# Optimization experiments

Measured on AMD Instinct MI355X. Metric: run time of the kernel, lower is better.

Reference implementation:

```python
import jax, jax.numpy as jnp
import numpy as np
from jax import lax

SEQ_SIZE = 4096
V = 4                               # vocab size
B = 256                             # batch
FILTER_SIZES = [4, 5, 6, 7, 8]
H = 10                              # lstm hidden
I = (len(FILTER_SIZES) + 1) * V     # lstm input size = 24


def setup_inputs() -> dict:
    key = jax.random.key(0)
    ks = jax.random.split(key, 9)
    inp = {"x": jax.random.normal(ks[0], (B, 1, V * SEQ_SIZE), dtype=jnp.float32)}
    for fs in FILTER_SIZES:
        # matches nn.init.constant_(conv.weight, 0.01)
        inp[f"w{fs}"] = jnp.full((1, 1, fs), 0.01, dtype=jnp.float32)
    s = 1.0 / float(np.sqrt(H))
    shapes = {"Wih": (4 * H, I), "Whh": (4 * H, H), "bih": (4 * H,), "bhh": (4 * H,)}
    k = 1
    for d in ("f", "r"):
        for nm, sh in shapes.items():
            inp[f"{nm}_{d}"] = jax.random.uniform(ks[k], sh, jnp.float32, -s, s)
            k += 1
    return inp


def _branch(x, w, fs):
    # x: (B,1,V*S); conv1d stride=V, VALID, no bias -> (B,1,L)
    conv = lax.conv_general_dilated(x, w, window_strides=(V,), padding="VALID",
                                    dimension_numbers=("NCH", "OIH", "NCH"))
    # winner_takes_all: (x + max_over_len)^2
    m = jnp.max(conv, axis=2, keepdims=True)
    v = ((conv + m) ** 2)[:, 0, :]                                  # (B,L)
    Bsz, L = v.shape
    # shape_convolutions2 == scatter-add of v[b,i] into out[b, V*i + j], j<fs
    idx = (V * jnp.arange(L)[:, None] + jnp.arange(fs)[None, :]).reshape(-1)
    contrib = jnp.broadcast_to(v[:, :, None], (Bsz, L, fs)).reshape(Bsz, -1)
    out = jnp.zeros((Bsz, V * SEQ_SIZE), v.dtype).at[:, idx].add(contrib)
    return out.reshape(Bsz, SEQ_SIZE, V)


def _lstm_dir(xs, Wih, Whh, bih, bhh, reverse):
    # xs: (S,B,I) -> hidden states (S,B,H), aligned with input positions
    Bsz = xs.shape[1]
    h0 = jnp.zeros((Bsz, H), xs.dtype)
    c0 = jnp.zeros((Bsz, H), xs.dtype)
    b = bih + bhh

    def step(carry, xt):
        h, c = carry
        g = xt @ Wih.T + h @ Whh.T + b          # (B,4H), torch gate order i,f,g,o
        i, f, gg, o = jnp.split(g, 4, axis=1)
        c = jax.nn.sigmoid(f) * c + jax.nn.sigmoid(i) * jnp.tanh(gg)
        h = jax.nn.sigmoid(o) * jnp.tanh(c)
        return (h, c), h

    _, hs = lax.scan(step, (h0, c0), xs, reverse=reverse)
    return hs


def _forward(x, ws, Wih_f, Whh_f, bih_f, bhh_f, Wih_r, Whh_r, bih_r, bhh_r):
    Bsz = x.shape[0]
    branches = [_branch(x, w, fs) for w, fs in zip(ws, FILTER_SIZES)]
    inp_r = x.reshape(Bsz, SEQ_SIZE, V)
    l_lstmin = jnp.concatenate(branches + [inp_r], axis=2)   # (B,S,24)
    xs = jnp.swapaxes(l_lstmin, 0, 1)                        # (S,B,24)
    hf = _lstm_dir(xs, Wih_f, Whh_f, bih_f, bhh_f, False)
    hr = _lstm_dir(xs, Wih_r, Whh_r, bih_r, bhh_r, True)
    h_sum = jnp.sum(hf, axis=2) + jnp.sum(hr, axis=2)        # (S,B)
    h_sum = h_sum.T                                          # (B,S)
    # l_in * repeated h_sum, reshaped and summed over vocab == inp_r * h_sum
    l_profile = jnp.sum(inp_r * h_sum[:, :, None], axis=2)   # (B,S)
    return jax.nn.sigmoid(jnp.sum(l_profile, axis=1, keepdims=True))  # (B,1)


def reference(x, w4, w5, w6, w7, w8, Wih_f, Whh_f, bih_f, bhh_f, Wih_r, Whh_r, bih_r, bhh_r):
    return _forward(x, [w4, w5, w6, w7, w8],
                    Wih_f, Whh_f, bih_f, bhh_f, Wih_r, Whh_r, bih_r, bhh_r)
```

## Files before the change

kernel.cpp:

```cpp
#include <hip/hip_runtime.h>

#define SEQ 4096
#define NBATCH 256

typedef float v2f __attribute__((ext_vector_type(2)));

__device__ __forceinline__ float sqf(float v) { return v * v; }
__device__ __forceinline__ float fexp2(float v) { return __builtin_amdgcn_exp2f(v); }
__device__ __forceinline__ float frcp(float v)  { return __builtin_amdgcn_rcpf(v); }

#define L2E 1.4426950408889634f

__device__ __forceinline__ unsigned fkey(float f) {
    const int b = __float_as_int(f);
    return (unsigned)(b ^ ((b >> 31) | 0x80000000));
}
__device__ __forceinline__ float fival(unsigned k) {
    const int b = (k & 0x80000000u) ? (int)(k ^ 0x80000000u) : (int)(~k);
    return __int_as_float(b);
}

__global__ void wprep_kernel(
    const float* __restrict__ Wih_f, const float* __restrict__ bih_f,
    const float* __restrict__ bhh_f,
    const float* __restrict__ Wih_r, const float* __restrict__ bih_r,
    const float* __restrict__ bhh_r,
    float* __restrict__ Wq, unsigned* __restrict__ MMu)
{
    const int t = threadIdx.x;
    for (int i = t; i < NBATCH * 5; i += 256) MMu[i] = 0u;
    if (t >= 80) return;
    const int d = t / 40, r = t % 40;
    const int gate = r / 10, unit = r % 10;
    const float* __restrict__ W  = (d ? Wih_r : Wih_f) + r * 24;
    const float* __restrict__ bi = d ? bih_r : bih_f;
    const float* __restrict__ bh = d ? bhh_r : bhh_f;
    const float sc = (gate == 2) ? (-2.f * L2E) : (-L2E);
    float o[13];
    o[0]  = W[0] + W[1] + W[2] + W[3];
    o[1]  = W[4] + W[5] + W[6] + W[7];
    o[2]  = W[4];
    o[3]  = W[8] + W[9] + W[10] + W[11];
    o[4]  = W[8] + W[9];
    o[5]  = W[12] + W[13] + W[14] + W[15];
    o[6]  = W[12] + W[13] + W[14];
    o[7]  = W[16] + W[17] + W[18] + W[19];
    o[8]  = W[20]; o[9] = W[21]; o[10] = W[22]; o[11] = W[23];
    o[12] = bi[r] + bh[r];
#pragma unroll
    for (int k = 0; k < 13; ++k)
        Wq[(((d * 10) + unit) * 13 + k) * 4 + gate] = o[k] * sc;
}

__global__ __launch_bounds__(256) void max_kernel(
    const float* __restrict__ x,
    const float* __restrict__ w4p, const float* __restrict__ w5p,
    const float* __restrict__ w6p, const float* __restrict__ w7p,
    const float* __restrict__ w8p,
    unsigned* __restrict__ MMu)
{
    const int b    = blockIdx.x >> 2;
    const int quar = blockIdx.x & 3;
    const int tid  = threadIdx.x;
    const float* __restrict__ xr = x + (size_t)b * (4 * SEQ);

    float W4[4], W5[5], W6[6], W7[7], W8[8];
#pragma unroll
    for (int k = 0; k < 4; ++k) W4[k] = w4p[k];
#pragma unroll
    for (int k = 0; k < 5; ++k) W5[k] = w5p[k];
#pragma unroll
    for (int k = 0; k < 6; ++k) W6[k] = w6p[k];
#pragma unroll
    for (int k = 0; k < 7; ++k) W7[k] = w7p[k];
#pragma unroll
    for (int k = 0; k < 8; ++k) W8[k] = w8p[k];

    float m4 = -3.4e38f, m5 = -3.4e38f, m6 = -3.4e38f, m7 = -3.4e38f, m8 = -3.4e38f;
    for (int i = quar * (SEQ / 4) + tid; i < (quar + 1) * (SEQ / 4); i += 256) {
        const float4 t0 = *reinterpret_cast<const float4*>(xr + 4 * i);
        const float xa0 = t0.x, xa1 = t0.y, xa2 = t0.z, xa3 = t0.w;
        const float c4 = xa0 * W4[0] + xa1 * W4[1] + xa2 * W4[2] + xa3 * W4[3];
        m4 = fmaxf(m4, c4);
        if (i < SEQ - 1) {
            const float4 t1 = *reinterpret_cast<const float4*>(xr + 4 * i + 4);
            const float xa4 = t1.x, xa5 = t1.y, xa6 = t1.z, xa7 = t1.w;
            const float c5 = xa0*W5[0]+xa1*W5[1]+xa2*W5[2]+xa3*W5[3]+xa4*W5[4];
            const float c6 = xa0*W6[0]+xa1*W6[1]+xa2*W6[2]+xa3*W6[3]+xa4*W6[4]+xa5*W6[5];
            const float c7 = xa0*W7[0]+xa1*W7[1]+xa2*W7[2]+xa3*W7[3]+xa4*W7[4]+xa5*W7[5]+xa6*W7[6];
            const float c8 = xa0*W8[0]+xa1*W8[1]+xa2*W8[2]+xa3*W8[3]+xa4*W8[4]+xa5*W8[5]+xa6*W8[6]+xa7*W8[7];
            m5 = fmaxf(m5, c5); m6 = fmaxf(m6, c6);
            m7 = fmaxf(m7, c7); m8 = fmaxf(m8, c8);
        }
    }
#pragma unroll
    for (int off = 32; off; off >>= 1) {
        m4 = fmaxf(m4, __shfl_down(m4, off));
        m5 = fmaxf(m5, __shfl_down(m5, off));
        m6 = fmaxf(m6, __shfl_down(m6, off));
        m7 = fmaxf(m7, __shfl_down(m7, off));
        m8 = fmaxf(m8, __shfl_down(m8, off));
    }
    __shared__ float wr[4][5];
    if ((tid & 63) == 0) {
        const int w = tid >> 6;
        wr[w][0] = m4; wr[w][1] = m5; wr[w][2] = m6; wr[w][3] = m7; wr[w][4] = m8;
    }
    __syncthreads();
    if (tid < 5) {
        const float m = fmaxf(fmaxf(wr[0][tid], wr[1][tid]),
                              fmaxf(wr[2][tid], wr[3][tid]));
        atomicMax(&MMu[b * 5 + tid], fkey(m));
    }
}

__global__ __launch_bounds__(256) void scatter_kernel(
    const float* __restrict__ x,
    const float* __restrict__ w4p, const float* __restrict__ w5p,
    const float* __restrict__ w6p, const float* __restrict__ w7p,
    const float* __restrict__ w8p,
    const unsigned* __restrict__ MMu,
    float* __restrict__ lin)
{
    const int b    = blockIdx.x >> 2;
    const int quar = blockIdx.x & 3;
    const int tid  = threadIdx.x;
    const float* __restrict__ xr = x + (size_t)b * (4 * SEQ);

    float W4[4], W5[5], W6[6], W7[7], W8[8];
#pragma unroll
    for (int k = 0; k < 4; ++k) W4[k] = w4p[k];
#pragma unroll
    for (int k = 0; k < 5; ++k) W5[k] = w5p[k];
#pragma unroll
    for (int k = 0; k < 6; ++k) W6[k] = w6p[k];
#pragma unroll
    for (int k = 0; k < 7; ++k) W7[k] = w7p[k];
#pragma unroll
    for (int k = 0; k < 8; ++k) W8[k] = w8p[k];

    const float M4 = fival(MMu[b * 5 + 0]), M5 = fival(MMu[b * 5 + 1]),
                M6 = fival(MMu[b * 5 + 2]), M7 = fival(MMu[b * 5 + 3]),
                M8 = fival(MMu[b * 5 + 4]);

    for (int s = quar * (SEQ / 4) + tid; s < (quar + 1) * (SEQ / 4); s += 256) {
        float xw[12];
        if (s > 0) {
            const float4 t = *reinterpret_cast<const float4*>(xr + 4 * s - 4);
            xw[0] = t.x; xw[1] = t.y; xw[2] = t.z; xw[3] = t.w;
        } else { xw[0] = xw[1] = xw[2] = xw[3] = 0.f; }
        {
            const float4 t = *reinterpret_cast<const float4*>(xr + 4 * s);
            xw[4] = t.x; xw[5] = t.y; xw[6] = t.z; xw[7] = t.w;
        }
        if (s < SEQ - 1) {
            const float4 t = *reinterpret_cast<const float4*>(xr + 4 * s + 4);
            xw[8] = t.x; xw[9] = t.y; xw[10] = t.z; xw[11] = t.w;
        } else { xw[8] = xw[9] = xw[10] = xw[11] = 0.f; }

        float c4s = 0.f, c5s = 0.f, c6s = 0.f, c7s = 0.f, c8s = 0.f;
        float c5p = 0.f, c6p = 0.f, c7p = 0.f, c8p = 0.f;
#pragma unroll
        for (int t = 0; t < 4; ++t) c4s += xw[4 + t] * W4[t];
#pragma unroll
        for (int t = 0; t < 5; ++t) { c5s += xw[4 + t] * W5[t]; c5p += xw[t] * W5[t]; }
#pragma unroll
        for (int t = 0; t < 6; ++t) { c6s += xw[4 + t] * W6[t]; c6p += xw[t] * W6[t]; }
#pragma unroll
        for (int t = 0; t < 7; ++t) { c7s += xw[4 + t] * W7[t]; c7p += xw[t] * W7[t]; }
#pragma unroll
        for (int t = 0; t < 8; ++t) { c8s += xw[4 + t] * W8[t]; c8p += xw[t] * W8[t]; }

        const bool oks = (s < SEQ - 1);
        const bool okp = (s > 0);
        const float v4s = sqf(c4s + M4);
        const float v5s = oks ? sqf(c5s + M5) : 0.f;
        const float v6s = oks ? sqf(c6s + M6) : 0.f;
        const float v7s = oks ? sqf(c7s + M7) : 0.f;
        const float v8s = oks ? sqf(c8s + M8) : 0.f;
        const float v5p = okp ? sqf(c5p + M5) : 0.f;
        const float v6p = okp ? sqf(c6p + M6) : 0.f;
        const float v7p = okp ? sqf(c7p + M7) : 0.f;
        const float v8p = okp ? sqf(c8p + M8) : 0.f;

        const float xsum = (xw[4] + xw[5]) + (xw[6] + xw[7]);
        float4* op = reinterpret_cast<float4*>(lin + ((size_t)b * SEQ + s) * 16);
        op[0] = make_float4(v4s, v5s, v5p, v6s);
        op[1] = make_float4(v6p, v7s, v7p, v8s + v8p);
        op[2] = make_float4(xw[4], xw[5], xw[6], xw[7]);
        op[3] = make_float4(xsum, 0.f, 0.f, 0.f);
    }
}

__global__ __launch_bounds__(64, 2) void lstm_kernel(
    const float* __restrict__ lin,
    const float* __restrict__ Wq,
    const float* __restrict__ Whh_f,
    const float* __restrict__ Whh_r,
    float* __restrict__ P)
{
    const int bg   = blockIdx.x & 63;
    const int d    = (blockIdx.x >> 6) & 1;
    const int q    = blockIdx.x >> 7;
    const int b0   = bg * 4;
    const int lane = threadIdx.x;

    const int s0 = q * 256 - 128;
    const int nChunks = 24, warmChunks = 8;

    __shared__ float vbuf[1024];
    __shared__ float hb[64];

    const int c   = lane >> 4;
    const int jr  = lane & 15;
    const int jc  = (jr < 10) ? jr : 0;

    hb[lane] = 0.f;

    v2f wINif[13], wINgo[13];
    {
        const float4* __restrict__ Wqp =
            reinterpret_cast<const float4*>(Wq) + (d * 10 + jc) * 13;
#pragma unroll
        for (int k = 0; k < 13; ++k) {
            const float4 w = Wqp[k];
            wINif[k] = (v2f){w.x, w.y};
            wINgo[k] = (v2f){w.z, w.w};
        }
    }
    const float* __restrict__ Whh = d ? Whh_r : Whh_f;
    v2f wIF[10], wGO[10];
#pragma unroll
    for (int k = 0; k < 10; ++k) {
        wIF[k] = (v2f){Whh[jc * 10 + k]        * (-L2E),
                       Whh[(10 + jc) * 10 + k] * (-L2E)};
        wGO[k] = (v2f){Whh[(20 + jc) * 10 + k] * (-2.f * L2E),
                       Whh[(30 + jc) * 10 + k] * (-L2E)};
    }

    const int lc = lane & 3;
    const int lr = lane >> 2;
    const float* __restrict__ chbase = lin + (size_t)(b0 + lc) * SEQ * 16;

    auto srcp = [&](int cn) {
        int sp = s0 + cn * 16 + lr;
        if (sp < 0) sp = 0;
        const int pos = d ? (SEQ - 1 - sp) : sp;
        return reinterpret_cast<const float4*>(chbase + (size_t)pos * 16);
    };

    float4 pR0, pR1, pR2, pR3;
    {
        const float4* a = srcp(0);
        pR0 = a[0]; pR1 = a[1]; pR2 = a[2]; pR3 = a[3];
    }

    float cs = 0.f, accS = 0.f;

    auto step = [&](int i) {
        const int ro = (i * 4 + c) * 4;
        const float4 q0 = *reinterpret_cast<const float4*>(&vbuf[ro]);
        const float4 q1 = *reinterpret_cast<const float4*>(&vbuf[256 + ro]);
        const float4 q2 = *reinterpret_cast<const float4*>(&vbuf[512 + ro]);
        const float  sx = vbuf[768 + ro];
        const float vv[12] = {q0.x, q0.y, q0.z, q0.w,
                              q1.x, q1.y, q1.z, q1.w,
                              q2.x, q2.y, q2.z, q2.w};
        v2f eI0 = wINif[12], eI1 = (v2f){0.f, 0.f};
        v2f eG0 = wINgo[12], eG1 = (v2f){0.f, 0.f};
#pragma unroll
        for (int k = 0; k < 12; k += 2) {
            const v2f v0 = (v2f){vv[k], vv[k]};
            const v2f v1 = (v2f){vv[k + 1], vv[k + 1]};
            eI0 += v0 * wINif[k]; eI1 += v1 * wINif[k + 1];
            eG0 += v0 * wINgo[k]; eG1 += v1 * wINgo[k + 1];
        }
        const v2f sIF = eI0 + eI1;
        const v2f sGO = eG0 + eG1;
        const float4 h03 = *reinterpret_cast<const float4*>(&hb[c * 16 + 0]);
        const float4 h47 = *reinterpret_cast<const float4*>(&hb[c * 16 + 4]);
        const float2 h89 = *reinterpret_cast<const float2*>(&hb[c * 16 + 8]);
        const float hj[10] = {h03.x, h03.y, h03.z, h03.w,
                              h47.x, h47.y, h47.z, h47.w, h89.x, h89.y};
        v2f eif0 = sIF, eif1 = (v2f){0.f, 0.f};
        v2f ego0 = sGO, ego1 = (v2f){0.f, 0.f};
#pragma unroll
        for (int k = 0; k < 10; k += 2) {
            const v2f h0 = (v2f){hj[k], hj[k]};
            const v2f h1 = (v2f){hj[k + 1], hj[k + 1]};
            eif0 += h0 * wIF[k]; eif1 += h1 * wIF[k + 1];
            ego0 += h0 * wGO[k]; ego1 += h1 * wGO[k + 1];
        }
        const v2f eif = eif0 + eif1, ego = ego0 + ego1;
        const float Ai = fexp2(eif.x);
        const float Fv = fexp2(eif.y);
        const float Bg = fexp2(fminf(ego.x, 80.f));
        const float Ov = fexp2(ego.y);
        const float sf = frcp(1.f + Fv);
        const float it = fmaf(Bg, 2.f * L2E, -2.f * L2E) *
                         frcp((1.f + Ai) * (1.f + Bg));
        cs = fmaf(sf, cs, it);
        const float Dv = fexp2(fminf(cs, 80.f));
        const float hv = (1.f - Dv) * frcp((1.f + Ov) * (1.f + Dv));
        hb[c * 16 + jr] = hv;
        accS = fmaf(sx, hv, accS);
    };

    for (int cn = 0; cn < nChunks; ++cn) {
        *reinterpret_cast<float4*>(&vbuf[lane * 4])       = pR0;
        *reinterpret_cast<float4*>(&vbuf[256 + lane * 4]) = pR1;
        *reinterpret_cast<float4*>(&vbuf[512 + lane * 4]) = pR2;
        *reinterpret_cast<float4*>(&vbuf[768 + lane * 4]) = pR3;
        asm volatile("s_waitcnt lgkmcnt(0)" ::: "memory");
        {
            const int nc = (cn + 1 < nChunks) ? cn + 1 : cn;
            const float4* a = srcp(nc);
            pR0 = a[0]; pR1 = a[1]; pR2 = a[2]; pR3 = a[3];
        }
#pragma unroll 4
        for (int i = 0; i < 16; ++i) step(i);
        if (cn + 1 == warmChunks) {
            accS = 0.f;
            if (q == 0) {
                cs = 0.f;
                hb[lane] = 0.f;
            }
        }
    }

    float vA = (jr < 10) ? accS : 0.f;
#pragma unroll
    for (int off = 1; off <= 8; off <<= 1) vA += __shfl_down(vA, off);
    if (jr == 0) P[q * 512 + d * 256 + b0 + c] = vA;
}

__global__ __launch_bounds__(256) void final_kernel(const float* __restrict__ P,
                                                    float* __restrict__ out)
{
    const int b = threadIdx.x;
    float v = 0.f;
#pragma unroll
    for (int seg = 0; seg < 16; ++seg)
        v += P[seg * 512 + b] + P[seg * 512 + 256 + b];
    out[b] = frcp(1.f + fexp2(-v * L2E));
}

extern "C" void kernel_launch(void* const* d_in, const int* in_sizes, int n_in,
                              void* d_out, int out_size, void* d_ws, size_t ws_size,
                              hipStream_t stream)
{
    const float* x     = (const float*)d_in[0];
    const float* w4    = (const float*)d_in[1];
    const float* w5    = (const float*)d_in[2];
    const float* w6    = (const float*)d_in[3];
    const float* w7    = (const float*)d_in[4];
    const float* w8    = (const float*)d_in[5];
    const float* Wih_f = (const float*)d_in[6];
    const float* Whh_f = (const float*)d_in[7];
    const float* bih_f = (const float*)d_in[8];
    const float* bhh_f = (const float*)d_in[9];
    const float* Wih_r = (const float*)d_in[10];
    const float* Whh_r = (const float*)d_in[11];
    const float* bih_r = (const float*)d_in[12];
    const float* bhh_r = (const float*)d_in[13];

    float*    lin = (float*)d_ws;
    float*    P   = lin + (size_t)NBATCH * SEQ * 16;
    unsigned* MMu = (unsigned*)(P + 8192);
    float*    Wqp = (float*)(MMu + 1280);

    wprep_kernel<<<1, 256, 0, stream>>>(Wih_f, bih_f, bhh_f,
                                        Wih_r, bih_r, bhh_r, Wqp, MMu);
    max_kernel<<<4 * NBATCH, 256, 0, stream>>>(x, w4, w5, w6, w7, w8, MMu);
    scatter_kernel<<<4 * NBATCH, 256, 0, stream>>>(x, w4, w5, w6, w7, w8, MMu, lin);
    lstm_kernel<<<2048, 64, 0, stream>>>(lin, Wqp, Whh_f, Whh_r, P);
    final_kernel<<<1, NBATCH, 0, stream>>>(P, (float*)d_out);
}
```

Baseline: 254.7 us.

## Fuse conv/scatter feature computation into LSTM kernel and drop weight-prep kernel

```diff
diff --git a/kernel.cpp b/kernel.cpp
--- a/kernel.cpp
+++ b/kernel.cpp
@@ -2,8 +2,6 @@
 
 #define SEQ 4096
 #define NBATCH 256
-
-typedef float v2f __attribute__((ext_vector_type(2)));
 
 __device__ __forceinline__ float sqf(float v) { return v * v; }
 __device__ __forceinline__ float fexp2(float v) { return __builtin_amdgcn_exp2f(v); }
@@ -18,38 +16,6 @@
 __device__ __forceinline__ float fival(unsigned k) {
     const int b = (k & 0x80000000u) ? (int)(k ^ 0x80000000u) : (int)(~k);
     return __int_as_float(b);
-}
-
-__global__ void wprep_kernel(
-    const float* __restrict__ Wih_f, const float* __restrict__ bih_f,
-    const float* __restrict__ bhh_f,
-    const float* __restrict__ Wih_r, const float* __restrict__ bih_r,
-    const float* __restrict__ bhh_r,
-    float* __restrict__ Wq, unsigned* __restrict__ MMu)
-{
-    const int t = threadIdx.x;
-    for (int i = t; i < NBATCH * 5; i += 256) MMu[i] = 0u;
-    if (t >= 80) return;
-    const int d = t / 40, r = t % 40;
-    const int gate = r / 10, unit = r % 10;
-    const float* __restrict__ W  = (d ? Wih_r : Wih_f) + r * 24;
-    const float* __restrict__ bi = d ? bih_r : bih_f;
-    const float* __restrict__ bh = d ? bhh_r : bhh_f;
-    const float sc = (gate == 2) ? (-2.f * L2E) : (-L2E);
-    float o[13];
-    o[0]  = W[0] + W[1] + W[2] + W[3];
-    o[1]  = W[4] + W[5] + W[6] + W[7];
-    o[2]  = W[4];
-    o[3]  = W[8] + W[9] + W[10] + W[11];
-    o[4]  = W[8] + W[9];
-    o[5]  = W[12] + W[13] + W[14] + W[15];
-    o[6]  = W[12] + W[13] + W[14];
-    o[7]  = W[16] + W[17] + W[18] + W[19];
-    o[8]  = W[20]; o[9] = W[21]; o[10] = W[22]; o[11] = W[23];
-    o[12] = bi[r] + bh[r];
-#pragma unroll
-    for (int k = 0; k < 13; ++k)
-        Wq[(((d * 10) + unit) * 13 + k) * 4 + gate] = o[k] * sc;
 }
 
 __global__ __launch_bounds__(256) void max_kernel(
@@ -114,89 +80,18 @@
     }
 }
 
-__global__ __launch_bounds__(256) void scatter_kernel(
+__global__ __launch_bounds__(64) __attribute__((amdgpu_waves_per_eu(2, 2)))
+void lstm_kernel(
     const float* __restrict__ x,
     const float* __restrict__ w4p, const float* __restrict__ w5p,
     const float* __restrict__ w6p, const float* __restrict__ w7p,
     const float* __restrict__ w8p,
     const unsigned* __restrict__ MMu,
-    float* __restrict__ lin)
-{
-    const int b    = blockIdx.x >> 2;
-    const int quar = blockIdx.x & 3;
-    const int tid  = threadIdx.x;
-    const float* __restrict__ xr = x + (size_t)b * (4 * SEQ);
-
-    float W4[4], W5[5], W6[6], W7[7], W8[8];
-#pragma unroll
-    for (int k = 0; k < 4; ++k) W4[k] = w4p[k];
-#pragma unroll
-    for (int k = 0; k < 5; ++k) W5[k] = w5p[k];
-#pragma unroll
-    for (int k = 0; k < 6; ++k) W6[k] = w6p[k];
-#pragma unroll
-    for (int k = 0; k < 7; ++k) W7[k] = w7p[k];
-#pragma unroll
-    for (int k = 0; k < 8; ++k) W8[k] = w8p[k];
-
-    const float M4 = fival(MMu[b * 5 + 0]), M5 = fival(MMu[b * 5 + 1]),
-                M6 = fival(MMu[b * 5 + 2]), M7 = fival(MMu[b * 5 + 3]),
-                M8 = fival(MMu[b * 5 + 4]);
-
-    for (int s = quar * (SEQ / 4) + tid; s < (quar + 1) * (SEQ / 4); s += 256) {
-        float xw[12];
-        if (s > 0) {
-            const float4 t = *reinterpret_cast<const float4*>(xr + 4 * s - 4);
-            xw[0] = t.x; xw[1] = t.y; xw[2] = t.z; xw[3] = t.w;
-        } else { xw[0] = xw[1] = xw[2] = xw[3] = 0.f; }
-        {
-            const float4 t = *reinterpret_cast<const float4*>(xr + 4 * s);
-            xw[4] = t.x; xw[5] = t.y; xw[6] = t.z; xw[7] = t.w;
-        }
-        if (s < SEQ - 1) {
-            const float4 t = *reinterpret_cast<const float4*>(xr + 4 * s + 4);
-            xw[8] = t.x; xw[9] = t.y; xw[10] = t.z; xw[11] = t.w;
-        } else { xw[8] = xw[9] = xw[10] = xw[11] = 0.f; }
-
-        float c4s = 0.f, c5s = 0.f, c6s = 0.f, c7s = 0.f, c8s = 0.f;
-        float c5p = 0.f, c6p = 0.f, c7p = 0.f, c8p = 0.f;
-#pragma unroll
-        for (int t = 0; t < 4; ++t) c4s += xw[4 + t] * W4[t];
-#pragma unroll
-        for (int t = 0; t < 5; ++t) { c5s += xw[4 + t] * W5[t]; c5p += xw[t] * W5[t]; }
-#pragma unroll
-        for (int t = 0; t < 6; ++t) { c6s += xw[4 + t] * W6[t]; c6p += xw[t] * W6[t]; }
-#pragma unroll
-        for (int t = 0; t < 7; ++t) { c7s += xw[4 + t] * W7[t]; c7p += xw[t] * W7[t]; }
-#pragma unroll
-        for (int t = 0; t < 8; ++t) { c8s += xw[4 + t] * W8[t]; c8p += xw[t] * W8[t]; }
-
-        const bool oks = (s < SEQ - 1);
-        const bool okp = (s > 0);
-        const float v4s = sqf(c4s + M4);
-        const float v5s = oks ? sqf(c5s + M5) : 0.f;
-        const float v6s = oks ? sqf(c6s + M6) : 0.f;
-        const float v7s = oks ? sqf(c7s + M7) : 0.f;
-        const float v8s = oks ? sqf(c8s + M8) : 0.f;
-        const float v5p = okp ? sqf(c5p + M5) : 0.f;
-        const float v6p = okp ? sqf(c6p + M6) : 0.f;
-        const float v7p = okp ? sqf(c7p + M7) : 0.f;
-        const float v8p = okp ? sqf(c8p + M8) : 0.f;
-
-        const float xsum = (xw[4] + xw[5]) + (xw[6] + xw[7]);
-        float4* op = reinterpret_cast<float4*>(lin + ((size_t)b * SEQ + s) * 16);
-        op[0] = make_float4(v4s, v5s, v5p, v6s);
-        op[1] = make_float4(v6p, v7s, v7p, v8s + v8p);
-        op[2] = make_float4(xw[4], xw[5], xw[6], xw[7]);
-        op[3] = make_float4(xsum, 0.f, 0.f, 0.f);
-    }
-}
-
-__global__ __launch_bounds__(64, 2) void lstm_kernel(
-    const float* __restrict__ lin,
-    const float* __restrict__ Wq,
-    const float* __restrict__ Whh_f,
-    const float* __restrict__ Whh_r,
+    const float* __restrict__ Wih_f, const float* __restrict__ bih_f,
+    const float* __restrict__ bhh_f,
+    const float* __restrict__ Wih_r, const float* __restrict__ bih_r,
+    const float* __restrict__ bhh_r,
+    const float* __restrict__ Whh_f, const float* __restrict__ Whh_r,
     float* __restrict__ P)
 {
     const int bg   = blockIdx.x & 63;
@@ -211,49 +106,88 @@
     __shared__ float vbuf[1024];
     __shared__ float hb[64];
 
-    const int c   = lane >> 4;
-    const int jr  = lane & 15;
-    const int jc  = (jr < 10) ? jr : 0;
+    const int c  = lane >> 4;
+    const int jr = lane & 15;
+    const int jc = (jr < 10) ? jr : 0;
 
     hb[lane] = 0.f;
 
-    v2f wINif[13], wINgo[13];
-    {
-        const float4* __restrict__ Wqp =
-            reinterpret_cast<const float4*>(Wq) + (d * 10 + jc) * 13;
-#pragma unroll
-        for (int k = 0; k < 13; ++k) {
-            const float4 w = Wqp[k];
-            wINif[k] = (v2f){w.x, w.y};
-            wINgo[k] = (v2f){w.z, w.w};
-        }
-    }
+    const float* __restrict__ Wih = d ? Wih_r : Wih_f;
+    const float* __restrict__ bi  = d ? bih_r : bih_f;
+    const float* __restrict__ bh  = d ? bhh_r : bhh_f;
+    float wI[13], wF[13], wG[13], wO[13];
+    auto fold = [&](int g, float sc, float* w) {
+        const int r = g * 10 + jc;
+        const float* __restrict__ W = Wih + r * 24;
+        w[0]  = (W[0] + W[1] + W[2] + W[3]) * sc;
+        w[1]  = (W[4] + W[5] + W[6] + W[7]) * sc;
+        w[2]  = W[4] * sc;
+        w[3]  = (W[8] + W[9] + W[10] + W[11]) * sc;
+        w[4]  = (W[8] + W[9]) * sc;
+        w[5]  = (W[12] + W[13] + W[14] + W[15]) * sc;
+        w[6]  = (W[12] + W[13] + W[14]) * sc;
+        w[7]  = (W[16] + W[17] + W[18] + W[19]) * sc;
+        w[8]  = W[20] * sc; w[9] = W[21] * sc;
+        w[10] = W[22] * sc; w[11] = W[23] * sc;
+        w[12] = (bi[r] + bh[r]) * sc;
+    };
+    fold(0, -L2E, wI); fold(1, -L2E, wF);
+    fold(2, -2.f * L2E, wG); fold(3, -L2E, wO);
+
     const float* __restrict__ Whh = d ? Whh_r : Whh_f;
-    v2f wIF[10], wGO[10];
+    float hI[10], hF[10], hG[10], hO[10];
 #pragma unroll
     for (int k = 0; k < 10; ++k) {
-        wIF[k] = (v2f){Whh[jc * 10 + k]        * (-L2E),
-                       Whh[(10 + jc) * 10 + k] * (-L2E)};
-        wGO[k] = (v2f){Whh[(20 + jc) * 10 + k] * (-2.f * L2E),
-                       Whh[(30 + jc) * 10 + k] * (-L2E)};
-    }
+        hI[k] = Whh[jc * 10 + k]        * (-L2E);
+        hF[k] = Whh[(10 + jc) * 10 + k] * (-L2E);
+        hG[k] = Whh[(20 + jc) * 10 + k] * (-2.f * L2E);
+        hO[k] = Whh[(30 + jc) * 10 + k] * (-L2E);
+    }
+#pragma unroll
+    for (int k = 0; k < 13; ++k)
+        asm volatile("" : "+v"(wI[k]), "+v"(wF[k]), "+v"(wG[k]), "+v"(wO[k]));
+#pragma unroll
+    for (int k = 0; k < 10; ++k)
+        asm volatile("" : "+v"(hI[k]), "+v"(hF[k]), "+v"(hG[k]), "+v"(hO[k]));
 
     const int lc = lane & 3;
     const int lr = lane >> 2;
-    const float* __restrict__ chbase = lin + (size_t)(b0 + lc) * SEQ * 16;
-
-    auto srcp = [&](int cn) {
+    const float* __restrict__ xr = x + (size_t)(b0 + lc) * (4 * SEQ);
+
+    float W4[4], W5[5], W6[6], W7[7], W8[8];
+#pragma unroll
+    for (int k = 0; k < 4; ++k) W4[k] = w4p[k];
+#pragma unroll
+    for (int k = 0; k < 5; ++k) W5[k] = w5p[k];
+#pragma unroll
+    for (int k = 0; k < 6; ++k) W6[k] = w6p[k];
+#pragma unroll
+    for (int k = 0; k < 7; ++k) W7[k] = w7p[k];
+#pragma unroll
+    for (int k = 0; k < 8; ++k) W8[k] = w8p[k];
+
+    const float M4 = fival(MMu[(b0 + lc) * 5 + 0]);
+    const float M5 = fival(MMu[(b0 + lc) * 5 + 1]);
+    const float M6 = fival(MMu[(b0 + lc) * 5 + 2]);
+    const float M7 = fival(MMu[(b0 + lc) * 5 + 3]);
+    const float M8 = fival(MMu[(b0 + lc) * 5 + 4]);
+
+    auto posof = [&](int cn) {
         int sp = s0 + cn * 16 + lr;
         if (sp < 0) sp = 0;
-        const int pos = d ? (SEQ - 1 - sp) : sp;
-        return reinterpret_cast<const float4*>(chbase + (size_t)pos * 16);
+        return d ? (SEQ - 1 - sp) : sp;
     };
-
-    float4 pR0, pR1, pR2, pR3;
-    {
-        const float4* a = srcp(0);
-        pR0 = a[0]; pR1 = a[1]; pR2 = a[2]; pR3 = a[3];
-    }
+    auto loadx = [&](int pos, float4& A, float4& B, float4& C) {
+        B = *reinterpret_cast<const float4*>(xr + 4 * pos);
+        A = (pos > 0) ? *reinterpret_cast<const float4*>(xr + 4 * pos - 4)
+                      : make_float4(0.f, 0.f, 0.f, 0.f);
+        C = (pos < SEQ - 1) ? *reinterpret_cast<const float4*>(xr + 4 * pos + 4)
+                            : make_float4(0.f, 0.f, 0.f, 0.f);
+    };
+
+    int posCur = posof(0);
+    float4 xA, xB, xC;
+    loadx(posCur, xA, xB, xC);
 
     float cs = 0.f, accS = 0.f;
 
@@ -266,36 +200,37 @@
         const float vv[12] = {q0.x, q0.y, q0.z, q0.w,
                               q1.x, q1.y, q1.z, q1.w,
                               q2.x, q2.y, q2.z, q2.w};
-        v2f eI0 = wINif[12], eI1 = (v2f){0.f, 0.f};
-        v2f eG0 = wINgo[12], eG1 = (v2f){0.f, 0.f};
-#pragma unroll
-        for (int k = 0; k < 12; k += 2) {
-            const v2f v0 = (v2f){vv[k], vv[k]};
-            const v2f v1 = (v2f){vv[k + 1], vv[k + 1]};
-            eI0 += v0 * wINif[k]; eI1 += v1 * wINif[k + 1];
-            eG0 += v0 * wINgo[k]; eG1 += v1 * wINgo[k + 1];
-        }
-        const v2f sIF = eI0 + eI1;
-        const v2f sGO = eG0 + eG1;
         const float4 h03 = *reinterpret_cast<const float4*>(&hb[c * 16 + 0]);
         const float4 h47 = *reinterpret_cast<const float4*>(&hb[c * 16 + 4]);
         const float2 h89 = *reinterpret_cast<const float2*>(&hb[c * 16 + 8]);
         const float hj[10] = {h03.x, h03.y, h03.z, h03.w,
                               h47.x, h47.y, h47.z, h47.w, h89.x, h89.y};
-        v2f eif0 = sIF, eif1 = (v2f){0.f, 0.f};
-        v2f ego0 = sGO, ego1 = (v2f){0.f, 0.f};
+        float ei0 = wI[12], ei1 = 0.f, ef0 = wF[12], ef1 = 0.f;
+        float eg0 = wG[12], eg1 = 0.f, eo0 = wO[12], eo1 = 0.f;
+#pragma unroll
+        for (int k = 0; k < 12; k += 2) {
+            ei0 = fmaf(vv[k], wI[k], ei0); ei1 = fmaf(vv[k + 1], wI[k + 1], ei1);
+            ef0 = fmaf(vv[k], wF[k], ef0); ef1 = fmaf(vv[k + 1], wF[k + 1], ef1);
+            eg0 = fmaf(vv[k], wG[k], eg0); eg1 = fmaf(vv[k + 1], wG[k + 1], eg1);
+            eo0 = fmaf(vv[k], wO[k], eo0); eo1 = fmaf(vv[k + 1], wO[k + 1], eo1);
+        }
+        const float si = ei0 + ei1, sf2 = ef0 + ef1;
+        const float sg = eg0 + eg1, so2 = eo0 + eo1;
+        float ai0 = si, ai1 = 0.f, af0 = sf2, af1 = 0.f;
+        float ag0 = sg, ag1 = 0.f, ao0 = so2, ao1 = 0.f;
 #pragma unroll
         for (int k = 0; k < 10; k += 2) {
-            const v2f h0 = (v2f){hj[k], hj[k]};
-            const v2f h1 = (v2f){hj[k + 1], hj[k + 1]};
-            eif0 += h0 * wIF[k]; eif1 += h1 * wIF[k + 1];
-            ego0 += h0 * wGO[k]; ego1 += h1 * wGO[k + 1];
-        }
-        const v2f eif = eif0 + eif1, ego = ego0 + ego1;
-        const float Ai = fexp2(eif.x);
-        const float Fv = fexp2(eif.y);
-        const float Bg = fexp2(fminf(ego.x, 80.f));
-        const float Ov = fexp2(ego.y);
+            ai0 = fmaf(hj[k], hI[k], ai0); ai1 = fmaf(hj[k + 1], hI[k + 1], ai1);
+            af0 = fmaf(hj[k], hF[k], af0); af1 = fmaf(hj[k + 1], hF[k + 1], af1);
+            ag0 = fmaf(hj[k], hG[k], ag0); ag1 = fmaf(hj[k + 1], hG[k + 1], ag1);
+            ao0 = fmaf(hj[k], hO[k], ao0); ao1 = fmaf(hj[k + 1], hO[k + 1], ao1);
+        }
+        const float eI = ai0 + ai1, eF = af0 + af1;
+        const float eG = ag0 + ag1, eO = ao0 + ao1;
+        const float Ai = fexp2(eI);
+        const float Fv = fexp2(eF);
+        const float Bg = fexp2(fminf(eG, 80.f));
+        const float Ov = fexp2(eO);
         const float sf = frcp(1.f + Fv);
         const float it = fmaf(Bg, 2.f * L2E, -2.f * L2E) *
                          frcp((1.f + Ai) * (1.f + Bg));
@@ -307,15 +242,50 @@
     };
 
     for (int cn = 0; cn < nChunks; ++cn) {
-        *reinterpret_cast<float4*>(&vbuf[lane * 4])       = pR0;
-        *reinterpret_cast<float4*>(&vbuf[256 + lane * 4]) = pR1;
-        *reinterpret_cast<float4*>(&vbuf[512 + lane * 4]) = pR2;
-        *reinterpret_cast<float4*>(&vbuf[768 + lane * 4]) = pR3;
+        {
+            const bool okp = posCur > 0, oks = posCur < SEQ - 1;
+            float xw[12];
+            xw[0] = xA.x; xw[1] = xA.y; xw[2]  = xA.z; xw[3]  = xA.w;
+            xw[4] = xB.x; xw[5] = xB.y; xw[6]  = xB.z; xw[7]  = xB.w;
+            xw[8] = xC.x; xw[9] = xC.y; xw[10] = xC.z; xw[11] = xC.w;
+
+            float c4s = 0.f, c5s = 0.f, c6s = 0.f, c7s = 0.f, c8s = 0.f;
+            float c5p = 0.f, c6p = 0.f, c7p = 0.f, c8p = 0.f;
+#pragma unroll
+            for (int t = 0; t < 4; ++t) c4s += xw[4 + t] * W4[t];
+#pragma unroll
+            for (int t = 0; t < 5; ++t) { c5s += xw[4 + t] * W5[t]; c5p += xw[t] * W5[t]; }
+#pragma unroll
+            for (int t = 0; t < 6; ++t) { c6s += xw[4 + t] * W6[t]; c6p += xw[t] * W6[t]; }
+#pragma unroll
+            for (int t = 0; t < 7; ++t) { c7s += xw[4 + t] * W7[t]; c7p += xw[t] * W7[t]; }
+#pragma unroll
+            for (int t = 0; t < 8; ++t) { c8s += xw[4 + t] * W8[t]; c8p += xw[t] * W8[t]; }
+
+            const float v4s = sqf(c4s + M4);
+            const float v5s = oks ? sqf(c5s + M5) : 0.f;
+            const float v6s = oks ? sqf(c6s + M6) : 0.f;
+            const float v7s = oks ? sqf(c7s + M7) : 0.f;
+            const float v8s = oks ? sqf(c8s + M8) : 0.f;
+            const float v5p = okp ? sqf(c5p + M5) : 0.f;
+            const float v6p = okp ? sqf(c6p + M6) : 0.f;
+            const float v7p = okp ? sqf(c7p + M7) : 0.f;
+            const float v8p = okp ? sqf(c8p + M8) : 0.f;
+            const float xsum = (xw[4] + xw[5]) + (xw[6] + xw[7]);
+
+            *reinterpret_cast<float4*>(&vbuf[lane * 4]) =
+                make_float4(v4s, v5s, v5p, v6s);
+            *reinterpret_cast<float4*>(&vbuf[256 + lane * 4]) =
+                make_float4(v6p, v7s, v7p, v8s + v8p);
+            *reinterpret_cast<float4*>(&vbuf[512 + lane * 4]) =
+                make_float4(xw[4], xw[5], xw[6], xw[7]);
+            vbuf[768 + lane * 4] = xsum;
+        }
         asm volatile("s_waitcnt lgkmcnt(0)" ::: "memory");
         {
             const int nc = (cn + 1 < nChunks) ? cn + 1 : cn;
-            const float4* a = srcp(nc);
-            pR0 = a[0]; pR1 = a[1]; pR2 = a[2]; pR3 = a[3];
+            posCur = posof(nc);
+            loadx(posCur, xA, xB, xC);
         }
 #pragma unroll 4
         for (int i = 0; i < 16; ++i) step(i);
@@ -364,15 +334,14 @@
     const float* bih_r = (const float*)d_in[12];
     const float* bhh_r = (const float*)d_in[13];
 
-    float*    lin = (float*)d_ws;
-    float*    P   = lin + (size_t)NBATCH * SEQ * 16;
+    float*    P   = (float*)d_ws;
     unsigned* MMu = (unsigned*)(P + 8192);
-    float*    Wqp = (float*)(MMu + 1280);
-
-    wprep_kernel<<<1, 256, 0, stream>>>(Wih_f, bih_f, bhh_f,
-                                        Wih_r, bih_r, bhh_r, Wqp, MMu);
+
+    hipMemsetAsync(MMu, 0, 1280 * sizeof(unsigned), stream);
     max_kernel<<<4 * NBATCH, 256, 0, stream>>>(x, w4, w5, w6, w7, w8, MMu);
-    scatter_kernel<<<4 * NBATCH, 256, 0, stream>>>(x, w4, w5, w6, w7, w8, MMu, lin);
-    lstm_kernel<<<2048, 64, 0, stream>>>(lin, Wqp, Whh_f, Whh_r, P);
+    lstm_kernel<<<2048, 64, 0, stream>>>(x, w4, w5, w6, w7, w8, MMu,
+                                         Wih_f, bih_f, bhh_f,
+                                         Wih_r, bih_r, bhh_r,
+                                         Whh_f, Whh_r, P);
     final_kernel<<<1, NBATCH, 0, stream>>>(P, (float*)d_out);
 }
```

New measurement: 244.8 us. -3.9%, faster.
